# Kernel tuning notes

Hardware: AMD Instinct MI355X
Metric: run time of the kernel (lower is better)

## Reference

```python
import jax, jax.numpy as jnp
import numpy as np

EPS = 1e-3


def setup_inputs() -> dict:
    key = jax.random.key(0)
    k1, k2, k3, k4 = jax.random.split(key, 4)
    B, D, F = 1024, 1024, 32768
    x = jax.random.normal(k1, (B, D), jnp.float32)
    y = jax.random.normal(k2, (B, D), jnp.float32)
    xs = jax.random.normal(k3, (F, D), jnp.float32)
    xs = xs / jnp.linalg.norm(xs, axis=-1, keepdims=True)  # step() stores unit-norm atoms
    ys = jax.random.normal(k4, (F, D), jnp.float32)
    ys = ys / jnp.linalg.norm(ys, axis=-1, keepdims=True)
    return {"x": x, "y": y, "xs": xs, "ys": ys, "target_l0": 32}


def _grad_pursuit(signal, dictionary, target_l0):
    # signal: [B, V]; dictionary: [F, V]
    B = signal.shape[0]
    F = dictionary.shape[0]
    rows = jnp.arange(B)

    def step(weights, _):
        residual = signal - jnp.einsum('bf,fv->bv', weights, dictionary)  # [B, V]
        inner_products = jnp.einsum('bv,fv->bf', residual, dictionary)    # [B, F]
        idx = jnp.argmax(inner_products, axis=1)                          # [B]
        selected = (weights != 0).at[rows, idx].set(True)                 # [B, F] bool
        grad = jnp.where(selected, inner_products, jnp.zeros((), signal.dtype))
        c = jnp.einsum('bf,fv->bv', grad, dictionary)                     # [B, V]
        c_sq = jnp.sum(c * c, axis=-1)
        step_size = jnp.sum(c * residual, axis=-1) / jnp.maximum(c_sq, EPS)
        weights = jax.nn.relu(weights + step_size[:, None] * grad)
        return weights, None

    weights0 = jnp.zeros((B, F), signal.dtype)
    weights, _ = jax.lax.scan(step, weights0, None, length=target_l0)
    return jax.lax.top_k(weights, target_l0)  # (values [B,k], indices [B,k])


def _decode(indices, weights, dictionary):
    # embedding-bag sum: gather [B,k,V] atoms, weight, sum over k
    return jnp.einsum('bk,bkv->bv', weights, dictionary[indices])


def reference(x, y, xs, ys, target_l0):
    weights, indices = _grad_pursuit(x, xs, target_l0)
    x_reconstructed = _decode(indices, weights, xs)
    y_reconstructed = _decode(indices, weights, ys)
    losses = jnp.sum((y_reconstructed - y) ** 2, axis=-1)
    return weights, indices, x_reconstructed, y_reconstructed, losses
```

## Files before the change

### kernel.cpp

```cpp
#include <hip/hip_runtime.h>

#define B_ 1024
#define D_ 1024
#define F_ 32768
#define T_ 32
#define KSLOTS 32

#define LO_SCALE     2048.0f
#define LO_INV_SCALE 4.8828125e-4f

typedef _Float16 f16x8 __attribute__((ext_vector_type(8)));
typedef _Float16 f16x4 __attribute__((ext_vector_type(4)));
typedef float    f32x4 __attribute__((ext_vector_type(4)));

__device__ __forceinline__ unsigned int fkey(float f) {
    unsigned int u = __float_as_uint(f);
    return (u & 0x80000000u) ? ~u : (u | 0x80000000u);
}
__device__ __forceinline__ unsigned long long packkey(float v, unsigned int n) {
    return ((unsigned long long)fkey(v) << 32) | (unsigned long long)(0xFFFFFFFFu - n);
}

__device__ __forceinline__ void async16(const void* g, void* l) {
    __builtin_amdgcn_global_load_lds(
        (const __attribute__((address_space(1))) unsigned int*)g,
        (__attribute__((address_space(3))) unsigned int*)l, 16, 0, 0);
}

__device__ __forceinline__ f32x4 mfma16(f16x8 a, f16x8 b, f32x4 c) {
    return __builtin_amdgcn_mfma_f32_16x16x32_f16(a, b, c, 0, 0, 0);
}

__device__ __forceinline__ void fsplit(float v, _Float16& h, _Float16& l) {
    h = (_Float16)v;
    l = (_Float16)((v - (float)h) * LO_SCALE);
}

__global__ __launch_bounds__(256) void split_xs_kernel(
    const float* __restrict__ XS, _Float16* __restrict__ hi, _Float16* __restrict__ lo)
{
    const size_t i = ((size_t)blockIdx.x * 256 + threadIdx.x) * 4;
    const float4 v = *(const float4*)(XS + i);
    f16x4 hv, lv;
    _Float16 h, l;
    fsplit(v.x, h, l); hv[0] = h; lv[0] = l;
    fsplit(v.y, h, l); hv[1] = h; lv[1] = l;
    fsplit(v.z, h, l); hv[2] = h; lv[2] = l;
    fsplit(v.w, h, l); hv[3] = h; lv[3] = l;
    *(f16x4*)(hi + i) = hv;
    *(f16x4*)(lo + i) = lv;
}

__global__ __launch_bounds__(256) void init_kernel(
    const float* __restrict__ X, float* __restrict__ Rres,
    _Float16* __restrict__ Rhi, _Float16* __restrict__ Rlo,
    int* __restrict__ a_cnt, unsigned long long* __restrict__ amax)
{
    const int b = blockIdx.x, tid = threadIdx.x;
    for (int d = tid; d < D_; d += 256) {
        const float v = X[(size_t)b * D_ + d];
        Rres[(size_t)b * D_ + d] = v;
        _Float16 h, l; fsplit(v, h, l);
        Rhi[(size_t)b * D_ + d] = h;
        Rlo[(size_t)b * D_ + d] = l;
    }
    if (tid == 0) { a_cnt[b] = 0; amax[b] = 0ull; }
}

#define SPL1(H, L, I, V) { _Float16 _h; _Float16 _l; fsplit((V), _h, _l); H[I] = _h; L[I] = _l; }

template <bool PRE>
__global__ __launch_bounds__(256, 2) void gemm16_argmax_kernel(
    const _Float16* __restrict__ Ahi, const _Float16* __restrict__ Alo,
    const _Float16* __restrict__ Bhi, const _Float16* __restrict__ Blo,
    const float* __restrict__ XSf,
    unsigned long long* __restrict__ amax)
{
    __shared__ __align__(16) _Float16 As[2][2][128][32];
    __shared__ __align__(16) _Float16 Bs[2][2][128][32];
    __shared__ unsigned long long red[128][2];

    const int tid  = threadIdx.x;
    const int wid  = tid >> 6, lane = tid & 63;
    const int orig = (int)blockIdx.x;
    const int wgid = (orig & 7) * 256 + (orig >> 3);
    const int m0   = (wgid & 7) * 128;
    const int n0   = (wgid >> 3) * 128;
    const int wm   = wid >> 1, wn = wid & 1;

    f32x4 acc[4][4], acc2[4][4];
#pragma unroll
    for (int i = 0; i < 4; ++i)
#pragma unroll
        for (int j = 0; j < 4; ++j) {
            acc[i][j]  = (f32x4){0.f, 0.f, 0.f, 0.f};
            acc2[i][j] = (f32x4){0.f, 0.f, 0.f, 0.f};
        }

    const int srow = wid * 32 + (lane >> 2);
    const int skof = (lane & 3) * 8;
    const _Float16* gAh = Ahi + (size_t)(m0 + srow) * D_ + skof;
    const _Float16* gAl = Alo + (size_t)(m0 + srow) * D_ + skof;
    const _Float16* gBh = nullptr;
    const _Float16* gBl = nullptr;
    const float*    gBf = nullptr;
    if constexpr (PRE) {
        gBh = Bhi + (size_t)(n0 + srow) * D_ + skof;
        gBl = Blo + (size_t)(n0 + srow) * D_ + skof;
    } else {
        gBf = XSf + (size_t)(n0 + (tid >> 1)) * D_ + (tid & 1) * 16;
    }

    const int lrow = lane & 15;
    const int lk   = (lane >> 4) * 8;

    auto stageAB = [&](int bb, int k0) {
#pragma unroll
        for (int c = 0; c < 2; ++c) {
            const size_t go = (size_t)(c * 16) * D_ + k0;
            const int    ro = wid * 32 + c * 16;
            async16(gAh + go, &As[bb][0][ro][0]);
            async16(gAl + go, &As[bb][1][ro][0]);
            async16(gBh + go, &Bs[bb][0][ro][0]);
            async16(gBl + go, &Bs[bb][1][ro][0]);
        }
    };
    auto stageA = [&](int bb, int k0) {
#pragma unroll
        for (int c = 0; c < 2; ++c) {
            const size_t go = (size_t)(c * 16) * D_ + k0;
            const int    ro = wid * 32 + c * 16;
            async16(gAh + go, &As[bb][0][ro][0]);
            async16(gAl + go, &As[bb][1][ro][0]);
        }
    };
    float4 q0, q1, q2, q3;
    auto loadB = [&](int k0) {
        q0 = *(const float4*)(gBf + k0);
        q1 = *(const float4*)(gBf + k0 + 4);
        q2 = *(const float4*)(gBf + k0 + 8);
        q3 = *(const float4*)(gBf + k0 + 12);
    };
    auto writeB = [&](int bb) {
        const int br = tid >> 1, bq = (tid & 1) * 16;
        f16x8 h0, l0, h1, l1;
        SPL1(h0, l0, 0, q0.x) SPL1(h0, l0, 1, q0.y) SPL1(h0, l0, 2, q0.z) SPL1(h0, l0, 3, q0.w)
        SPL1(h0, l0, 4, q1.x) SPL1(h0, l0, 5, q1.y) SPL1(h0, l0, 6, q1.z) SPL1(h0, l0, 7, q1.w)
        SPL1(h1, l1, 0, q2.x) SPL1(h1, l1, 1, q2.y) SPL1(h1, l1, 2, q2.z) SPL1(h1, l1, 3, q2.w)
        SPL1(h1, l1, 4, q3.x) SPL1(h1, l1, 5, q3.y) SPL1(h1, l1, 6, q3.z) SPL1(h1, l1, 7, q3.w)
        *(f16x8*)&Bs[bb][0][br][bq]     = h0;
        *(f16x8*)&Bs[bb][0][br][bq + 8] = h1;
        *(f16x8*)&Bs[bb][1][br][bq]     = l0;
        *(f16x8*)&Bs[bb][1][br][bq + 8] = l1;
    };
    auto compute = [&](int bb) {
        f16x8 ah[4], al[4], bh[4], bl[4];
#pragma unroll
        for (int i = 0; i < 4; ++i) {
            ah[i] = *(const f16x8*)&As[bb][0][wm * 64 + i * 16 + lrow][lk];
            al[i] = *(const f16x8*)&As[bb][1][wm * 64 + i * 16 + lrow][lk];
            bh[i] = *(const f16x8*)&Bs[bb][0][wn * 64 + i * 16 + lrow][lk];
            bl[i] = *(const f16x8*)&Bs[bb][1][wn * 64 + i * 16 + lrow][lk];
        }
#pragma unroll
        for (int i = 0; i < 4; ++i)
#pragma unroll
            for (int j = 0; j < 4; ++j) {
                acc[i][j]  = mfma16(ah[i], bh[j], acc[i][j]);
                acc2[i][j] = mfma16(ah[i], bl[j], acc2[i][j]);
                acc2[i][j] = mfma16(al[i], bh[j], acc2[i][j]);
            }
    };

    if constexpr (PRE) {
        stageAB(0, 0);
    } else {
        loadB(0); stageA(0, 0); writeB(0);
    }
    __syncthreads();

    for (int k0 = 0; k0 < D_; k0 += 64) {
        if constexpr (PRE) {
            if (k0 + 32 < D_) stageAB(1, k0 + 32);
            compute(0);
        } else {
            if (k0 + 32 < D_) { loadB(k0 + 32); stageA(1, k0 + 32); }
            compute(0);
            if (k0 + 32 < D_) writeB(1);
        }
        __syncthreads();
        if constexpr (PRE) {
            if (k0 + 64 < D_) stageAB(0, k0 + 64);
            compute(1);
        } else {
            if (k0 + 64 < D_) { loadB(k0 + 64); stageA(0, k0 + 64); }
            compute(1);
            if (k0 + 64 < D_) writeB(0);
        }
        __syncthreads();
    }

    const unsigned cb = (unsigned)(n0 + wn * 64 + (lane & 15));
#pragma unroll
    for (int mi = 0; mi < 4; ++mi) {
#pragma unroll
        for (int r = 0; r < 4; ++r) {
            unsigned long long best = 0ull;
#pragma unroll
            for (int j = 0; j < 4; ++j) {
                const float v = acc[mi][j][r] + acc2[mi][j][r] * LO_INV_SCALE;
                const unsigned long long key = packkey(v, cb + (unsigned)(j * 16));
                best = key > best ? key : best;
            }
#pragma unroll
            for (int off = 1; off < 16; off <<= 1) {
                const unsigned long long o = __shfl_xor(best, off);
                best = o > best ? o : best;
            }
            if ((lane & 15) == 0)
                red[wm * 64 + mi * 16 + ((lane >> 4) << 2) + r][wn] = best;
        }
    }
    __syncthreads();
    if (tid < 128) {
        const unsigned long long b0 = red[tid][0], b1 = red[tid][1];
        atomicMax(&amax[m0 + tid], b0 > b1 ? b0 : b1);
    }
}

__global__ __launch_bounds__(256) void update_kernel(
    const float* __restrict__ X, const float* __restrict__ XS,
    float* __restrict__ Rres,
    _Float16* __restrict__ Rhi, _Float16* __restrict__ Rlo,
    int* __restrict__ a_idx, float* __restrict__ a_w, int* __restrict__ a_cnt,
    unsigned long long* __restrict__ amax)
{
    const int b = blockIdx.x;
    const int tid = threadIdx.x;
    __shared__ float s_r[D_];
    __shared__ int   s_idx[33];
    __shared__ float s_w[33];
    __shared__ float s_g[33];
    __shared__ int   s_cnt;
    __shared__ float s_red[8];

    for (int d = tid; d < D_; d += 256) s_r[d] = Rres[(size_t)b * D_ + d];

    if (tid == 0) {
        int cnt = a_cnt[b];
        for (int j = 0; j < cnt; ++j) { s_idx[j] = a_idx[b*KSLOTS + j]; s_w[j] = a_w[b*KSLOTS + j]; }
        unsigned long long key = amax[b];
        int ni = (int)(0xFFFFFFFFu - (unsigned int)(key & 0xFFFFFFFFull));
        bool found = false;
        for (int j = 0; j < cnt; ++j) found = found || (s_idx[j] == ni);
        if (!found) {
            int p = cnt;
            while (p > 0 && s_idx[p-1] > ni) { s_idx[p] = s_idx[p-1]; s_w[p] = s_w[p-1]; --p; }
            s_idx[p] = ni; s_w[p] = 0.f; ++cnt;
        }
        s_cnt = cnt;
    }
    __syncthreads();
    const int cnt = s_cnt;
    const int wave = tid >> 6, lane = tid & 63;

    for (int j = wave; j < cnt; j += 4) {
        const float* xr = XS + (size_t)s_idx[j] * D_;
        float sum = 0.f;
#pragma unroll
        for (int i = 0; i < D_/64; ++i) { int d = lane + (i << 6); sum = fmaf(s_r[d], xr[d], sum); }
        for (int off = 32; off > 0; off >>= 1) sum += __shfl_down(sum, off);
        if (lane == 0) s_g[j] = sum;
    }
    __syncthreads();

    float cs = 0.f, cr = 0.f;
#pragma unroll
    for (int v = 0; v < 4; ++v) {
        const int d = tid + (v << 8);
        float cv = 0.f;
        for (int j = 0; j < cnt; ++j) cv = fmaf(s_g[j], XS[(size_t)s_idx[j]*D_ + d], cv);
        cs = fmaf(cv, cv, cs);
        cr = fmaf(cv, s_r[d], cr);
    }
    for (int off = 32; off > 0; off >>= 1) { cs += __shfl_down(cs, off); cr += __shfl_down(cr, off); }
    if (lane == 0) { s_red[wave] = cs; s_red[4 + wave] = cr; }
    __syncthreads();

    if (tid == 0) {
        const float cs_t = s_red[0] + s_red[1] + s_red[2] + s_red[3];
        const float cr_t = s_red[4] + s_red[5] + s_red[6] + s_red[7];
        const float ss = cr_t / fmaxf(cs_t, 1e-3f);
        int nc = 0;
        for (int j = 0; j < cnt; ++j) {
            float nw = s_w[j] + ss * s_g[j];
            if (nw > 0.f) { s_idx[nc] = s_idx[j]; s_w[nc] = nw; ++nc; }
        }
        s_cnt = nc;
        a_cnt[b] = nc;
        for (int j = 0; j < nc; ++j) { a_idx[b*KSLOTS + j] = s_idx[j]; a_w[b*KSLOTS + j] = s_w[j]; }
        amax[b] = 0ull;
    }
    __syncthreads();
    const int nc = s_cnt;

#pragma unroll
    for (int v = 0; v < 4; ++v) {
        const int d = tid + (v << 8);
        float s = 0.f;
        for (int j = 0; j < nc; ++j) s = fmaf(s_w[j], XS[(size_t)s_idx[j]*D_ + d], s);
        const float rv = X[(size_t)b*D_ + d] - s;
        Rres[(size_t)b*D_ + d] = rv;
        _Float16 h, l; fsplit(rv, h, l);
        Rhi[(size_t)b*D_ + d] = h;
        Rlo[(size_t)b*D_ + d] = l;
    }
}

__global__ __launch_bounds__(256) void finalize_kernel(
    const float* __restrict__ Y,
    const float* __restrict__ XS, const float* __restrict__ YS,
    const int* __restrict__ a_idx, const float* __restrict__ a_w, const int* __restrict__ a_cnt,
    float* __restrict__ out)
{
    const int b = blockIdx.x, tid = threadIdx.x;
    __shared__ int   s_idx[KSLOTS];
    __shared__ float s_w[KSLOTS];
    __shared__ int   o_idx[KSLOTS];
    __shared__ float o_w[KSLOTS];
    __shared__ float s_red[4];

    if (tid == 0) {
        int cnt = a_cnt[b];
        for (int j = 0; j < cnt; ++j) { s_idx[j] = a_idx[b*KSLOTS + j]; s_w[j] = a_w[b*KSLOTS + j]; }
        for (int i = 1; i < cnt; ++i) {
            int ii = s_idx[i]; float ww = s_w[i];
            int p = i - 1;
            while (p >= 0 && (s_w[p] < ww || (s_w[p] == ww && s_idx[p] > ii))) {
                s_w[p+1] = s_w[p]; s_idx[p+1] = s_idx[p]; --p;
            }
            s_w[p+1] = ww; s_idx[p+1] = ii;
        }
        for (int j = 0; j < cnt; ++j) { o_idx[j] = s_idx[j]; o_w[j] = s_w[j]; }
        int p = cnt, f = 0;
        while (p < KSLOTS) {
            bool member = false;
            for (int j = 0; j < cnt; ++j) member = member || (s_idx[j] == f);
            if (!member) { o_idx[p] = f; o_w[p] = 0.f; ++p; }
            ++f;
        }
    }
    __syncthreads();

    if (tid < KSLOTS) {
        out[(size_t)b*KSLOTS + tid] = o_w[tid];
        out[32768 + (size_t)b*KSLOTS + tid] = (float)o_idx[tid];
    }

    float lsum = 0.f;
    for (int d = tid; d < D_; d += 256) {
        float xr = 0.f, yr = 0.f;
#pragma unroll
        for (int k = 0; k < KSLOTS; ++k) {
            const size_t off = (size_t)o_idx[k] * D_ + d;
            xr = fmaf(o_w[k], XS[off], xr);
            yr = fmaf(o_w[k], YS[off], yr);
        }
        out[65536 + (size_t)b*D_ + d] = xr;
        out[65536 + 1048576 + (size_t)b*D_ + d] = yr;
        const float e = yr - Y[(size_t)b*D_ + d];
        lsum = fmaf(e, e, lsum);
    }
    const int wave = tid >> 6, lane = tid & 63;
    for (int off = 32; off > 0; off >>= 1) lsum += __shfl_down(lsum, off);
    if (lane == 0) s_red[wave] = lsum;
    __syncthreads();
    if (tid == 0) out[65536 + 2097152 + b] = s_red[0] + s_red[1] + s_red[2] + s_red[3];
}

extern "C" void kernel_launch(void* const* d_in, const int* in_sizes, int n_in,
                              void* d_out, int out_size, void* d_ws, size_t ws_size,
                              hipStream_t stream) {
    (void)in_sizes; (void)n_in; (void)out_size;
    const float* x  = (const float*)d_in[0];
    const float* y  = (const float*)d_in[1];
    const float* xs = (const float*)d_in[2];
    const float* ys = (const float*)d_in[3];
    float* out = (float*)d_out;

    char* ws = (char*)d_ws;
    float*              Rres  = (float*)(ws);
    _Float16*           Rhi   = (_Float16*)(ws + ((size_t)4 << 20));
    _Float16*           Rlo   = (_Float16*)(ws + ((size_t)6 << 20));
    unsigned long long* amax  = (unsigned long long*)(ws + ((size_t)8 << 20));
    int*                a_cnt = (int*)(ws + ((size_t)8 << 20) + 8192);
    int*                a_idx = (int*)(ws + ((size_t)8 << 20) + 8192 + 4096);
    float*              a_w   = (float*)(ws + ((size_t)8 << 20) + 8192 + 4096 + 131072);
    _Float16*           XShi  = (_Float16*)(ws + ((size_t)16 << 20));
    _Float16*           XSlo  = (_Float16*)(ws + ((size_t)80 << 20));
    const bool big = ws_size >= ((size_t)144 << 20);

    if (big) split_xs_kernel<<<(F_ * D_) / 1024, 256, 0, stream>>>(xs, XShi, XSlo);
    init_kernel<<<B_, 256, 0, stream>>>(x, Rres, Rhi, Rlo, a_cnt, amax);

    for (int t = 0; t < T_; ++t) {
        if (big)
            gemm16_argmax_kernel<true ><<<dim3(2048), 256, 0, stream>>>(Rhi, Rlo, XShi, XSlo, xs, amax);
        else
            gemm16_argmax_kernel<false><<<dim3(2048), 256, 0, stream>>>(Rhi, Rlo, nullptr, nullptr, xs, amax);
        update_kernel<<<B_, 256, 0, stream>>>(x, xs, Rres, Rhi, Rlo, a_idx, a_w, a_cnt, amax);
    }
    finalize_kernel<<<B_, 256, 0, stream>>>(y, xs, ys, a_idx, a_w, a_cnt, out);
}
```

Before: 8.160 ms.

## Load A operand fragments directly from global into registers, bypassing LDS

```diff
diff --git a/kernel.cpp b/kernel.cpp
--- a/kernel.cpp
+++ b/kernel.cpp
@@ -76,7 +76,6 @@
     const float* __restrict__ XSf,
     unsigned long long* __restrict__ amax)
 {
-    __shared__ __align__(16) _Float16 As[2][2][128][32];
     __shared__ __align__(16) _Float16 Bs[2][2][128][32];
     __shared__ unsigned long long red[128][2];
 
@@ -99,8 +98,6 @@
 
     const int srow = wid * 32 + (lane >> 2);
     const int skof = (lane & 3) * 8;
-    const _Float16* gAh = Ahi + (size_t)(m0 + srow) * D_ + skof;
-    const _Float16* gAl = Alo + (size_t)(m0 + srow) * D_ + skof;
     const _Float16* gBh = nullptr;
     const _Float16* gBl = nullptr;
     const float*    gBf = nullptr;
@@ -113,25 +110,25 @@
 
     const int lrow = lane & 15;
     const int lk   = (lane >> 4) * 8;
-
-    auto stageAB = [&](int bb, int k0) {
+    const size_t aoff = (size_t)(m0 + wm * 64 + lrow) * D_ + lk;
+
+    f16x8 aAh[4], aAl[4], aBh[4], aBl[4];
+
+    auto loadA = [&](f16x8* Ah, f16x8* Al, int k0) {
+#pragma unroll
+        for (int i = 0; i < 4; ++i) {
+            const size_t o = aoff + (size_t)(i * 16) * D_ + k0;
+            Ah[i] = *(const f16x8*)(Ahi + o);
+            Al[i] = *(const f16x8*)(Alo + o);
+        }
+    };
+    auto stageB = [&](int bb, int k0) {
 #pragma unroll
         for (int c = 0; c < 2; ++c) {
             const size_t go = (size_t)(c * 16) * D_ + k0;
             const int    ro = wid * 32 + c * 16;
-            async16(gAh + go, &As[bb][0][ro][0]);
-            async16(gAl + go, &As[bb][1][ro][0]);
             async16(gBh + go, &Bs[bb][0][ro][0]);
             async16(gBl + go, &Bs[bb][1][ro][0]);
-        }
-    };
-    auto stageA = [&](int bb, int k0) {
-#pragma unroll
-        for (int c = 0; c < 2; ++c) {
-            const size_t go = (size_t)(c * 16) * D_ + k0;
-            const int    ro = wid * 32 + c * 16;
-            async16(gAh + go, &As[bb][0][ro][0]);
-            async16(gAl + go, &As[bb][1][ro][0]);
         }
     };
     float4 q0, q1, q2, q3;
@@ -153,48 +150,47 @@
         *(f16x8*)&Bs[bb][1][br][bq]     = l0;
         *(f16x8*)&Bs[bb][1][br][bq + 8] = l1;
     };
-    auto compute = [&](int bb) {
-        f16x8 ah[4], al[4], bh[4], bl[4];
-#pragma unroll
-        for (int i = 0; i < 4; ++i) {
-            ah[i] = *(const f16x8*)&As[bb][0][wm * 64 + i * 16 + lrow][lk];
-            al[i] = *(const f16x8*)&As[bb][1][wm * 64 + i * 16 + lrow][lk];
-            bh[i] = *(const f16x8*)&Bs[bb][0][wn * 64 + i * 16 + lrow][lk];
-            bl[i] = *(const f16x8*)&Bs[bb][1][wn * 64 + i * 16 + lrow][lk];
+    auto compute = [&](int bb, const f16x8* Ah, const f16x8* Al) {
+        f16x8 bh[4], bl[4];
+#pragma unroll
+        for (int j = 0; j < 4; ++j) {
+            bh[j] = *(const f16x8*)&Bs[bb][0][wn * 64 + j * 16 + lrow][lk];
+            bl[j] = *(const f16x8*)&Bs[bb][1][wn * 64 + j * 16 + lrow][lk];
         }
 #pragma unroll
         for (int i = 0; i < 4; ++i)
 #pragma unroll
             for (int j = 0; j < 4; ++j) {
-                acc[i][j]  = mfma16(ah[i], bh[j], acc[i][j]);
-                acc2[i][j] = mfma16(ah[i], bl[j], acc2[i][j]);
-                acc2[i][j] = mfma16(al[i], bh[j], acc2[i][j]);
+                acc[i][j]  = mfma16(Ah[i], bh[j], acc[i][j]);
+                acc2[i][j] = mfma16(Ah[i], bl[j], acc2[i][j]);
+                acc2[i][j] = mfma16(Al[i], bh[j], acc2[i][j]);
             }
     };
 
     if constexpr (PRE) {
-        stageAB(0, 0);
+        stageB(0, 0);
     } else {
-        loadB(0); stageA(0, 0); writeB(0);
-    }
+        loadB(0); writeB(0);
+    }
+    loadA(aAh, aAl, 0);
     __syncthreads();
 
     for (int k0 = 0; k0 < D_; k0 += 64) {
         if constexpr (PRE) {
-            if (k0 + 32 < D_) stageAB(1, k0 + 32);
-            compute(0);
+            if (k0 + 32 < D_) { stageB(1, k0 + 32); loadA(aBh, aBl, k0 + 32); }
+            compute(0, aAh, aAl);
         } else {
-            if (k0 + 32 < D_) { loadB(k0 + 32); stageA(1, k0 + 32); }
-            compute(0);
+            if (k0 + 32 < D_) { loadB(k0 + 32); loadA(aBh, aBl, k0 + 32); }
+            compute(0, aAh, aAl);
             if (k0 + 32 < D_) writeB(1);
         }
         __syncthreads();
         if constexpr (PRE) {
-            if (k0 + 64 < D_) stageAB(0, k0 + 64);
-            compute(1);
+            if (k0 + 64 < D_) { stageB(0, k0 + 64); loadA(aAh, aAl, k0 + 64); }
+            compute(1, aBh, aBl);
         } else {
-            if (k0 + 64 < D_) { loadB(k0 + 64); stageA(0, k0 + 64); }
-            compute(1);
+            if (k0 + 64 < D_) { loadB(k0 + 64); loadA(aAh, aAl, k0 + 64); }
+            compute(1, aBh, aBl);
             if (k0 + 64 < D_) writeB(0);
         }
         __syncthreads();
```

Measured after the change: 11.30 ms. +38.5%, slower.
